# Kernel optimization log

Measured on AMD Instinct MI355X. Metric: run time of the kernel, lower is better.

The kernel has to match this reference:

```python
import jax, jax.numpy as jnp
import numpy as np

N_NODES = 50000
N_EDGES = 800000
N_GRAPHS = 64
F_IN = 128
HID = 64
HEADS = 4
N_CLS = 10
NEG_SLOPE = 0.2


def _glorot(key, shape):
    fan_in, fan_out = shape[-1], shape[-2] if len(shape) > 1 else shape[-1]
    lim = jnp.sqrt(6.0 / (fan_in + fan_out))
    return jax.random.uniform(key, shape, jnp.float32, -lim, lim)


def setup_inputs() -> dict:
    key = jax.random.key(0)
    ks = jax.random.split(key, 20)
    x = jax.random.normal(ks[0], (N_NODES, F_IN), jnp.float32)
    edge_index = jax.random.randint(ks[1], (2, N_EDGES), 0, N_NODES, jnp.int32)
    batch = jnp.sort(jax.random.randint(ks[2], (N_NODES,), 0, N_GRAPHS, jnp.int32))
    HC = HID * HEADS
    return {
        "x": x, "edge_index": edge_index, "batch": batch,
        # node embedding Linear(F_IN -> HID)
        "W_emb": _glorot(ks[3], (HID, F_IN)), "b_emb": jnp.zeros((HID,), jnp.float32),
        # gat1: HID -> HID, heads=4, concat
        "W1": _glorot(ks[4], (HC, HID)),
        "a_src1": _glorot(ks[5], (HEADS, HID)), "a_dst1": _glorot(ks[6], (HEADS, HID)),
        "b1": jnp.zeros((HC,), jnp.float32),
        # gat2: HC -> HID, heads=4, concat
        "W2": _glorot(ks[7], (HC, HC)),
        "a_src2": _glorot(ks[8], (HEADS, HID)), "a_dst2": _glorot(ks[9], (HEADS, HID)),
        "b2": jnp.zeros((HC,), jnp.float32),
        # gat3: HC -> HID, heads=1, mean
        "W3": _glorot(ks[10], (HID, HC)),
        "a_src3": _glorot(ks[11], (1, HID)), "a_dst3": _glorot(ks[12], (1, HID)),
        "b3": jnp.zeros((HID,), jnp.float32),
        # classifier: Linear(2*HID -> HID), ReLU, Linear(HID -> N_CLS)
        "Wc1": _glorot(ks[13], (HID, 2 * HID)), "bc1": jnp.zeros((HID,), jnp.float32),
        "Wc2": _glorot(ks[14], (N_CLS, HID)), "bc2": jnp.zeros((N_CLS,), jnp.float32),
    }


def _gat_layer(x, src, dst, W, a_src, a_dst, b, concat):
    """PyG-style GATConv (eval mode, self-loops already in src/dst)."""
    N = x.shape[0]
    H, C = a_src.shape
    h = (x @ W.T).reshape(N, H, C)                       # [N,H,C]
    s = jnp.einsum("nhc,hc->nh", h, a_src)               # [N,H]
    d = jnp.einsum("nhc,hc->nh", h, a_dst)               # [N,H]
    e = jax.nn.leaky_relu(s[src] + d[dst], NEG_SLOPE)    # [E,H]
    emax = jax.lax.stop_gradient(jax.ops.segment_max(e, dst, num_segments=N))
    emax = jnp.where(jnp.isfinite(emax), emax, 0.0)
    ex = jnp.exp(e - emax[dst])
    den = jax.ops.segment_sum(ex, dst, num_segments=N)   # [N,H]
    alpha = ex / (den[dst] + 1e-16)                      # segment softmax
    out = jax.ops.segment_sum(h[src] * alpha[:, :, None], dst, num_segments=N)
    out = out.reshape(N, H * C) if concat else out.mean(axis=1)
    return out + b


def reference(x, edge_index, batch, W_emb, b_emb, W1, a_src1, a_dst1, b1,
              W2, a_src2, a_dst2, b2, W3, a_src3, a_dst3, b3, Wc1, bc1, Wc2, bc2):
    N = x.shape[0]
    loops = jnp.arange(N, dtype=edge_index.dtype)
    src = jnp.concatenate([edge_index[0], loops])
    dst = jnp.concatenate([edge_index[1], loops])

    h = x @ W_emb.T + b_emb
    h = jax.nn.elu(_gat_layer(h, src, dst, W1, a_src1, a_dst1, b1, True))
    h = jax.nn.elu(_gat_layer(h, src, dst, W2, a_src2, a_dst2, b2, True))
    h = jax.nn.elu(_gat_layer(h, src, dst, W3, a_src3, a_dst3, b3, False))

    counts = jax.ops.segment_sum(jnp.ones((N,), h.dtype), batch, num_segments=N_GRAPHS)
    mean = jax.ops.segment_sum(h, batch, num_segments=N_GRAPHS) / jnp.maximum(counts, 1.0)[:, None]
    mx = jax.ops.segment_max(h, batch, num_segments=N_GRAPHS)
    mx = jnp.where(counts[:, None] > 0, mx, 0.0)
    g = jnp.concatenate([mean, mx], axis=1)              # [B, 2*HID]

    g = jax.nn.relu(g @ Wc1.T + bc1)
    return g @ Wc2.T + bc2                               # [B, N_CLS]
```

## Files before the change

kernel.cpp:

```cpp
#include <hip/hip_runtime.h>
#include <math.h>

#define NG 64
#define F_IN 128
#define NEG_SLOPE 0.2f

typedef __attribute__((ext_vector_type(8))) short s16x8;
typedef __attribute__((ext_vector_type(4))) float f32x4;

static __device__ __forceinline__ float elu_f(float x) { return x > 0.f ? x : expm1f(x); }
static __device__ __forceinline__ float lrelu(float x) { return x > 0.f ? x : NEG_SLOPE * x; }
static __device__ __forceinline__ unsigned enc_f32(float x) {
    unsigned u = __float_as_uint(x);
    return (u & 0x80000000u) ? ~u : (u | 0x80000000u);
}
static __device__ __forceinline__ float dec_f32(unsigned u) {
    unsigned b = (u & 0x80000000u) ? (u & 0x7fffffffu) : ~u;
    return __uint_as_float(b);
}
static __device__ __forceinline__ unsigned short bf16_rn(float x) {
    unsigned u = __float_as_uint(x);
    unsigned r = u + 0x7FFFu + ((u >> 16) & 1u);
    return (unsigned short)(r >> 16);
}
static __device__ __forceinline__ float bf16_to_f32(unsigned short h) {
    return __uint_as_float(((unsigned)h) << 16);
}
static __device__ __forceinline__ unsigned pack_split(float x) {
    unsigned short hi = bf16_rn(x);
    unsigned short lo = bf16_rn(x - bf16_to_f32(hi));
    return ((unsigned)hi << 16) | lo;
}

__global__ void convert_pack(const float* __restrict__ in, unsigned* __restrict__ out, int n) {
    int idx = (blockIdx.x * blockDim.x + threadIdx.x) * 4;
    if (idx + 3 < n) {
        float4 v = *(const float4*)&in[idx];
        uint4 o;
        o.x = pack_split(v.x); o.y = pack_split(v.y);
        o.z = pack_split(v.z); o.w = pack_split(v.w);
        *(uint4*)&out[idx] = o;
    }
}

__global__ void convert_dual(const float* __restrict__ in, unsigned short* __restrict__ hi,
                             unsigned short* __restrict__ lo, int n) {
    int idx = (blockIdx.x * blockDim.x + threadIdx.x) * 4;
    if (idx + 3 < n) {
        float4 v = *(const float4*)&in[idx];
        ushort4 h, l;
        h.x = bf16_rn(v.x); l.x = bf16_rn(v.x - bf16_to_f32(h.x));
        h.y = bf16_rn(v.y); l.y = bf16_rn(v.y - bf16_to_f32(h.y));
        h.z = bf16_rn(v.z); l.z = bf16_rn(v.z - bf16_to_f32(h.z));
        h.w = bf16_rn(v.w); l.w = bf16_rn(v.w - bf16_to_f32(h.w));
        *(ushort4*)&hi[idx] = h;
        *(ushort4*)&lo[idx] = l;
    }
}

__global__ void uvec_kernel(const float* __restrict__ W1, const float* __restrict__ a1s,
                            const float* __restrict__ a1d,
                            float* __restrict__ us, float* __restrict__ ud) {
    int h = threadIdx.x >> 6;
    int i = threadIdx.x & 63;
    float s = 0.f, d = 0.f;
    for (int o = 0; o < 64; ++o) {
        float w = W1[(h * 64 + o) * 64 + i];
        s = fmaf(w, a1s[h * 64 + o], s);
        d = fmaf(w, a1d[h * 64 + o], d);
    }
    us[h * 64 + i] = s;
    ud[h * 64 + i] = d;
}

__global__ void hist_kernel(const int* __restrict__ ei, int* __restrict__ cnt, int E, int N) {
    int e = blockIdx.x * blockDim.x + threadIdx.x;
    int ET = E + N;
    if (e >= ET) return;
    int dst = (e < E) ? ei[E + e] : (e - E);
    atomicAdd(&cnt[dst], 1);
}

__global__ void scan1_kernel(const int* __restrict__ cnt, int* __restrict__ excl,
                             int* __restrict__ bsum, int n) {
    __shared__ int sm[256];
    int t = threadIdx.x;
    int base = blockIdx.x * 1024 + t * 4;
    int v[4];
    #pragma unroll
    for (int u = 0; u < 4; ++u) { int idx = base + u; v[u] = (idx < n) ? cnt[idx] : 0; }
    int tsum = v[0] + v[1] + v[2] + v[3];
    sm[t] = tsum;
    __syncthreads();
    for (int off = 1; off < 256; off <<= 1) {
        int y = (t >= off) ? sm[t - off] : 0;
        __syncthreads();
        sm[t] += y;
        __syncthreads();
    }
    int run = sm[t] - tsum;
    #pragma unroll
    for (int u = 0; u < 4; ++u) {
        int idx = base + u;
        if (idx < n) excl[idx] = run;
        run += v[u];
    }
    if (t == 255) bsum[blockIdx.x] = sm[255];
}

__global__ void scan2_kernel(int* __restrict__ bsum, int* __restrict__ offs, int nb, int n) {
    if (blockIdx.x == 0 && threadIdx.x == 0) {
        int run = 0;
        for (int b = 0; b < nb; ++b) { int t = bsum[b]; bsum[b] = run; run += t; }
        offs[n] = run;
    }
}

__global__ void scan3_kernel(int* __restrict__ offs, const int* __restrict__ bsum, int n) {
    int base = blockIdx.x * 1024 + threadIdx.x * 4;
    int add = bsum[blockIdx.x];
    #pragma unroll
    for (int u = 0; u < 4; ++u) { int idx = base + u; if (idx < n) offs[idx] += add; }
}

__global__ void scatter_kernel(const int* __restrict__ ei, const int* __restrict__ offs,
                               int* __restrict__ cursor, int* __restrict__ csr_src, int E, int N) {
    int e = blockIdx.x * blockDim.x + threadIdx.x;
    int ET = E + N;
    if (e >= ET) return;
    int src, dst;
    if (e < E) { src = ei[e]; dst = ei[E + e]; }
    else       { src = e - E; dst = e - E; }
    int pos = offs[dst] + atomicAdd(&cursor[dst], 1);
    csr_src[pos] = src;
}

template<int K, int BN, int HATT, bool SHARED, bool SLICED, bool DO_ELU, int OUTM>
__global__ __launch_bounds__(256) void gemm_nolds(const unsigned* __restrict__ Ap, int lda,
                                                  const unsigned short* __restrict__ Whi,
                                                  const unsigned short* __restrict__ Wlo,
                                                  void* __restrict__ OutV, int M,
                                                  const float* __restrict__ bias,
                                                  const float* __restrict__ asrc,
                                                  const float* __restrict__ adst,
                                                  float* __restrict__ S, float* __restrict__ D,
                                                  int N) {
    constexpr int RF = (BN == 256) ? 4 : 1;
    constexpr int CF = 4;
    const int t = threadIdx.x;
    const int lane = t & 63;
    const int w = t >> 6;
    const int lj = lane & 15;
    const int kg = lane >> 4;
    const int n0 = blockIdx.x * 64;
    const int m0 = blockIdx.y * BN;
    const int rbase = (BN == 256) ? 0 : w * 16;
    const int cbase = (BN == 256) ? w * 64 : 0;
    const int aoff = SLICED ? blockIdx.y * K : 0;
    const unsigned short* __restrict__ WhiB = SLICED ? Whi + (size_t)blockIdx.y * BN * K : Whi;
    const unsigned short* __restrict__ WloB = SLICED ? Wlo + (size_t)blockIdx.y * BN * K : Wlo;

    f32x4 acc[RF][CF];
    #pragma unroll
    for (int rf = 0; rf < RF; ++rf)
        #pragma unroll
        for (int cf = 0; cf < CF; ++cf) acc[rf][cf] = (f32x4){0.f, 0.f, 0.f, 0.f};

    for (int kc = 0; kc < K; kc += 32) {
        s16x8 ah[RF], al[RF];
        #pragma unroll
        for (int rf = 0; rf < RF; ++rf) {
            int row = n0 + rbase + rf * 16 + lj;
            unsigned p[8];
            if (row < N) {
                uint4 q0 = *(const uint4*)&Ap[(size_t)row * lda + aoff + kc + kg * 8];
                uint4 q1 = *(const uint4*)&Ap[(size_t)row * lda + aoff + kc + kg * 8 + 4];
                p[0] = q0.x; p[1] = q0.y; p[2] = q0.z; p[3] = q0.w;
                p[4] = q1.x; p[5] = q1.y; p[6] = q1.z; p[7] = q1.w;
            } else {
                #pragma unroll
                for (int i = 0; i < 8; ++i) p[i] = 0;
            }
            #pragma unroll
            for (int i = 0; i < 8; ++i) {
                ah[rf][i] = (short)(p[i] >> 16);
                al[rf][i] = (short)(p[i] & 0xffffu);
            }
        }
        #pragma unroll
        for (int cf = 0; cf < CF; ++cf) {
            int wcol = (SLICED ? 0 : m0) + cbase + cf * 16 + lj;
            s16x8 bh = *(const s16x8*)&WhiB[(size_t)wcol * K + kc + kg * 8];
            s16x8 bl = *(const s16x8*)&WloB[(size_t)wcol * K + kc + kg * 8];
            #pragma unroll
            for (int rf = 0; rf < RF; ++rf) {
                acc[rf][cf] = __builtin_amdgcn_mfma_f32_16x16x32_bf16(ah[rf], bh, acc[rf][cf], 0, 0, 0);
                acc[rf][cf] = __builtin_amdgcn_mfma_f32_16x16x32_bf16(ah[rf], bl, acc[rf][cf], 0, 0, 0);
                acc[rf][cf] = __builtin_amdgcn_mfma_f32_16x16x32_bf16(al[rf], bh, acc[rf][cf], 0, 0, 0);
            }
        }
    }

    #pragma unroll
    for (int cf = 0; cf < CF; ++cf) {
        int gcol = m0 + cbase + cf * 16 + lj;
        float bv = bias ? bias[gcol] : 0.f;
        #pragma unroll
        for (int rf = 0; rf < RF; ++rf) {
            #pragma unroll
            for (int r = 0; r < 4; ++r) {
                int gn = n0 + rbase + rf * 16 + (lane >> 4) * 4 + r;
                if (gn < N) {
                    float o = acc[rf][cf][r] + bv;
                    if (DO_ELU) o = elu_f(o);
                    if (OUTM == 0)      ((float*)OutV)[(size_t)gn * M + gcol] = o;
                    else if (OUTM == 1) ((unsigned short*)OutV)[(size_t)gn * M + gcol] = bf16_rn(o);
                    else                ((unsigned*)OutV)[(size_t)gn * M + gcol] = pack_split(o);
                }
            }
        }
    }
    if (HATT > 0) {
        if (BN == 256) {
            float aw[CF], dw[CF], bw[CF];
            #pragma unroll
            for (int cf = 0; cf < CF; ++cf) {
                aw[cf] = asrc[w * 64 + cf * 16 + lj];
                dw[cf] = adst[w * 64 + cf * 16 + lj];
                bw[cf] = bias ? bias[m0 + cbase + cf * 16 + lj] : 0.f;
            }
            #pragma unroll
            for (int rf = 0; rf < RF; ++rf) {
                #pragma unroll
                for (int r = 0; r < 4; ++r) {
                    float sp = 0.f, dp = 0.f;
                    #pragma unroll
                    for (int cf = 0; cf < CF; ++cf) {
                        float vv = acc[rf][cf][r] + bw[cf];
                        sp = fmaf(vv, aw[cf], sp);
                        dp = fmaf(vv, dw[cf], dp);
                    }
                    #pragma unroll
                    for (int off = 1; off < 16; off <<= 1) {
                        sp += __shfl_xor(sp, off);
                        dp += __shfl_xor(dp, off);
                    }
                    if (lj == 0) {
                        int gn = n0 + rf * 16 + (lane >> 4) * 4 + r;
                        if (gn < N) { S[gn * HATT + w] = sp; D[gn * HATT + w] = dp; }
                    }
                }
            }
        } else {
            #pragma unroll
            for (int hh = 0; hh < HATT; ++hh) {
                float aw[CF], dw[CF], bw[CF];
                #pragma unroll
                for (int c2 = 0; c2 < CF; ++c2) {
                    aw[c2] = asrc[hh * 64 + c2 * 16 + lj];
                    dw[c2] = adst[hh * 64 + c2 * 16 + lj];
                    bw[c2] = bias ? bias[m0 + c2 * 16 + lj] : 0.f;
                }
                #pragma unroll
                for (int r = 0; r < 4; ++r) {
                    float sp = 0.f, dp = 0.f;
                    #pragma unroll
                    for (int c2 = 0; c2 < CF; ++c2) {
                        float vv = acc[0][c2][r] + bw[c2];
                        sp = fmaf(vv, aw[c2], sp);
                        dp = fmaf(vv, dw[c2], dp);
                    }
                    #pragma unroll
                    for (int off = 1; off < 16; off <<= 1) {
                        sp += __shfl_xor(sp, off);
                        dp += __shfl_xor(dp, off);
                    }
                    if (lj == 0) {
                        int gn = n0 + w * 16 + (lane >> 4) * 4 + r;
                        if (gn < N) { S[gn * HATT + hh] = sp; D[gn * HATT + hh] = dp; }
                    }
                }
            }
        }
    }
}

__global__ __launch_bounds__(256, 8) void gat_agg_x(const float* __restrict__ xA,
                                                    const float* __restrict__ s,
                                                    const float* __restrict__ d,
                                                    const int* __restrict__ offs,
                                                    const int* __restrict__ csr_src,
                                                    unsigned* __restrict__ G,
                                                    int N) {
    __shared__ float stash[4][64 * 5];
    int wv = threadIdx.x >> 6;
    int lane = threadIdx.x & 63;
    int node = (blockIdx.x * blockDim.x + threadIdx.x) >> 6;
    if (node >= N) return;
    float* st = stash[wv];
    int e0 = offs[node], e1 = offs[node + 1];
    float4 dv4 = *(const float4*)&d[node * 4];
    float dd[4] = {dv4.x, dv4.y, dv4.z, dv4.w};
    float mrun[4] = {-INFINITY, -INFINITY, -INFINITY, -INFINITY};
    float den[4] = {0.f, 0.f, 0.f, 0.f};
    float acc[4] = {0.f, 0.f, 0.f, 0.f};

    for (int base = e0; base < e1; base += 64) {
        int cnt = min(64, e1 - base);
        float ev[4] = {-INFINITY, -INFINITY, -INFINITY, -INFINITY};
        if (lane < cnt) {
            int src = csr_src[base + lane];
            float4 sv = *(const float4*)&s[src * 4];
            ev[0] = lrelu(sv.x + dd[0]); ev[1] = lrelu(sv.y + dd[1]);
            ev[2] = lrelu(sv.z + dd[2]); ev[3] = lrelu(sv.w + dd[3]);
            st[lane * 5 + 0] = ev[0]; st[lane * 5 + 1] = ev[1];
            st[lane * 5 + 2] = ev[2]; st[lane * 5 + 3] = ev[3];
            st[lane * 5 + 4] = __int_as_float(src);
        }
        #pragma unroll
        for (int h = 0; h < 4; ++h) {
            float m = ev[h];
            #pragma unroll
            for (int off = 32; off; off >>= 1) m = fmaxf(m, __shfl_xor(m, off));
            float mnew = fmaxf(mrun[h], m);
            float scale = __expf(mrun[h] - mnew);
            acc[h] *= scale; den[h] *= scale;
            mrun[h] = mnew;
        }
        int k = 0;
        for (; k + 4 <= cnt; k += 4) {
            int si[4];
            #pragma unroll
            for (int u = 0; u < 4; ++u) si[u] = __float_as_int(st[(k + u) * 5 + 4]);
            float vx[4];
            #pragma unroll
            for (int u = 0; u < 4; ++u) vx[u] = xA[(size_t)si[u] * 64 + lane];
            #pragma unroll
            for (int u = 0; u < 4; ++u) {
                #pragma unroll
                for (int h = 0; h < 4; ++h) {
                    float p = __expf(st[(k + u) * 5 + h] - mrun[h]);
                    den[h] += p;
                    acc[h] = fmaf(p, vx[u], acc[h]);
                }
            }
        }
        for (; k < cnt; ++k) {
            int src = __float_as_int(st[k * 5 + 4]);
            float v = xA[(size_t)src * 64 + lane];
            #pragma unroll
            for (int h = 0; h < 4; ++h) {
                float p = __expf(st[k * 5 + h] - mrun[h]);
                den[h] += p;
                acc[h] = fmaf(p, v, acc[h]);
            }
        }
    }
    #pragma unroll
    for (int h = 0; h < 4; ++h)
        G[(size_t)node * 256 + h * 64 + lane] = pack_split(acc[h] / (den[h] + 1e-16f));
}

template<int H, bool OUTPACK>
__global__ __launch_bounds__(256, 8) void gat_agg(const unsigned short* __restrict__ hp,
                                                  const float* __restrict__ s,
                                                  const float* __restrict__ d,
                                                  const int* __restrict__ offs,
                                                  const int* __restrict__ csr_src,
                                                  const float* __restrict__ bias,
                                                  void* __restrict__ outV, int N) {
    const int SW = (H == 4) ? 5 : 2;
    __shared__ float stash[4][64 * 5];
    int wv = threadIdx.x >> 6;
    int lane = threadIdx.x & 63;
    int node = (blockIdx.x * blockDim.x + threadIdx.x) >> 6;
    if (node >= N) return;
    float* st = stash[wv];
    int e0 = offs[node], e1 = offs[node + 1];

    float dd[H];
    #pragma unroll
    for (int h = 0; h < H; ++h) dd[h] = d[node * H + h];

    const int hd = (H == 4) ? (lane >> 4) : 0;

    float mrun = -INFINITY;
    float acc0 = 0.f, acc1 = 0.f, acc2 = 0.f, acc3 = 0.f, den = 0.f;

    for (int base = e0; base < e1; base += 64) {
        int cnt = min(64, e1 - base);
        float ev[H];
        #pragma unroll
        for (int h = 0; h < H; ++h) ev[h] = -INFINITY;
        if (lane < cnt) {
            int src = csr_src[base + lane];
            if (H == 4) {
                float4 sv = *(const float4*)&s[src * 4];
                ev[0] = lrelu(sv.x + dd[0]); ev[1] = lrelu(sv.y + dd[1]);
                ev[2] = lrelu(sv.z + dd[2]); ev[3] = lrelu(sv.w + dd[3]);
                st[lane * 5 + 0] = ev[0]; st[lane * 5 + 1] = ev[1];
                st[lane * 5 + 2] = ev[2]; st[lane * 5 + 3] = ev[3];
                st[lane * 5 + 4] = __int_as_float(src);
            } else {
                ev[0] = lrelu(s[src] + dd[0]);
                st[lane * 2 + 0] = ev[0];
                st[lane * 2 + 1] = __int_as_float(src);
            }
        }
        float mc[H];
        #pragma unroll
        for (int h = 0; h < H; ++h) {
            float m = ev[h];
            #pragma unroll
            for (int off = 32; off; off >>= 1) m = fmaxf(m, __shfl_xor(m, off));
            mc[h] = m;
        }
        float mch = mc[0];
        if (H == 4)
            mch = (lane & 32) ? ((lane & 16) ? mc[3] : mc[2]) : ((lane & 16) ? mc[1] : mc[0]);
        float mnew = fmaxf(mrun, mch);
        float scale = __expf(mrun - mnew);
        acc0 *= scale; acc1 *= scale; acc2 *= scale; acc3 *= scale; den *= scale;
        mrun = mnew;

        int k = 0;
        for (; k + 4 <= cnt; k += 4) {
            float ea = st[(k + 0) * SW + hd];
            float eb = st[(k + 1) * SW + hd];
            float ec = st[(k + 2) * SW + hd];
            float ed = st[(k + 3) * SW + hd];
            int sa = __float_as_int(st[(k + 0) * SW + SW - 1]);
            int sb = __float_as_int(st[(k + 1) * SW + SW - 1]);
            int sc = __float_as_int(st[(k + 2) * SW + SW - 1]);
            int sd_ = __float_as_int(st[(k + 3) * SW + SW - 1]);
            float pa = __expf(ea - mrun);
            float pb = __expf(eb - mrun);
            float pc = __expf(ec - mrun);
            float pd = __expf(ed - mrun);
            den += (pa + pb) + (pc + pd);
            if (H == 4) {
                uint2 ua = *(const uint2*)&hp[(size_t)sa * 256 + lane * 4];
                uint2 ub = *(const uint2*)&hp[(size_t)sb * 256 + lane * 4];
                uint2 uc = *(const uint2*)&hp[(size_t)sc * 256 + lane * 4];
                uint2 ud = *(const uint2*)&hp[(size_t)sd_ * 256 + lane * 4];
                acc0 = fmaf(pa, __uint_as_float((ua.x & 0xffffu) << 16), acc0);
                acc1 = fmaf(pa, __uint_as_float(ua.x & 0xffff0000u), acc1);
                acc2 = fmaf(pa, __uint_as_float((ua.y & 0xffffu) << 16), acc2);
                acc3 = fmaf(pa, __uint_as_float(ua.y & 0xffff0000u), acc3);
                acc0 = fmaf(pb, __uint_as_float((ub.x & 0xffffu) << 16), acc0);
                acc1 = fmaf(pb, __uint_as_float(ub.x & 0xffff0000u), acc1);
                acc2 = fmaf(pb, __uint_as_float((ub.y & 0xffffu) << 16), acc2);
                acc3 = fmaf(pb, __uint_as_float(ub.y & 0xffff0000u), acc3);
                acc0 = fmaf(pc, __uint_as_float((uc.x & 0xffffu) << 16), acc0);
                acc1 = fmaf(pc, __uint_as_float(uc.x & 0xffff0000u), acc1);
                acc2 = fmaf(pc, __uint_as_float((uc.y & 0xffffu) << 16), acc2);
                acc3 = fmaf(pc, __uint_as_float(uc.y & 0xffff0000u), acc3);
                acc0 = fmaf(pd, __uint_as_float((ud.x & 0xffffu) << 16), acc0);
                acc1 = fmaf(pd, __uint_as_float(ud.x & 0xffff0000u), acc1);
                acc2 = fmaf(pd, __uint_as_float((ud.y & 0xffffu) << 16), acc2);
                acc3 = fmaf(pd, __uint_as_float(ud.y & 0xffff0000u), acc3);
            } else {
                float ha = bf16_to_f32(hp[(size_t)sa * 64 + lane]);
                float hb = bf16_to_f32(hp[(size_t)sb * 64 + lane]);
                float hc = bf16_to_f32(hp[(size_t)sc * 64 + lane]);
                float hdv = bf16_to_f32(hp[(size_t)sd_ * 64 + lane]);
                acc0 = fmaf(pa, ha, acc0);
                acc0 = fmaf(pb, hb, acc0);
                acc0 = fmaf(pc, hc, acc0);
                acc0 = fmaf(pd, hdv, acc0);
            }
        }
        for (; k < cnt; ++k) {
            float e = st[k * SW + hd];
            int src = __float_as_int(st[k * SW + SW - 1]);
            float p = __expf(e - mrun);
            den += p;
            if (H == 4) {
                uint2 uv = *(const uint2*)&hp[(size_t)src * 256 + lane * 4];
                acc0 = fmaf(p, __uint_as_float((uv.x & 0xffffu) << 16), acc0);
                acc1 = fmaf(p, __uint_as_float(uv.x & 0xffff0000u), acc1);
                acc2 = fmaf(p, __uint_as_float((uv.y & 0xffffu) << 16), acc2);
                acc3 = fmaf(p, __uint_as_float(uv.y & 0xffff0000u), acc3);
            } else {
                acc0 = fmaf(p, bf16_to_f32(hp[(size_t)src * 64 + lane]), acc0);
            }
        }
    }

    float inv = 1.0f / (den + 1e-16f);
    if (H == 4) {
        float4 bv = *(const float4*)&bias[lane * 4];
        float o0 = elu_f(acc0 * inv + bv.x);
        float o1 = elu_f(acc1 * inv + bv.y);
        float o2 = elu_f(acc2 * inv + bv.z);
        float o3 = elu_f(acc3 * inv + bv.w);
        if (OUTPACK) {
            uint4 q;
            q.x = pack_split(o0); q.y = pack_split(o1);
            q.z = pack_split(o2); q.w = pack_split(o3);
            *(uint4*)&((unsigned*)outV)[(size_t)node * 256 + lane * 4] = q;
        } else {
            float4 o = make_float4(o0, o1, o2, o3);
            *(float4*)&((float*)outV)[(size_t)node * 256 + lane * 4] = o;
        }
    } else {
        float o = elu_f(acc0 * inv + bias[lane]);
        if (OUTPACK) ((unsigned*)outV)[(size_t)node * 64 + lane] = pack_split(o);
        else         ((float*)outV)[(size_t)node * 64 + lane] = o;
    }
}

__global__ void pool_init(float* gsum, unsigned* gmax, int* gcnt) {
    int t = blockIdx.x * blockDim.x + threadIdx.x;
    if (t < NG * 64) { gsum[t] = 0.f; gmax[t] = enc_f32(-INFINITY); }
    if (t < NG) gcnt[t] = 0;
}

__global__ void pool_reduce(const float* __restrict__ h3, const int* __restrict__ batch,
                            float* __restrict__ gsum, unsigned* __restrict__ gmax,
                            int* __restrict__ gcnt, int N, int per) {
    int w = (blockIdx.x * blockDim.x + threadIdx.x) >> 6;
    int lane = threadIdx.x & 63;
    int n0 = w * per;
    int n1 = min(N, n0 + per);
    float lsum = 0.f, lmax = -INFINITY;
    int cur = -1, cnt = 0;
    for (int n = n0; n < n1; ++n) {
        int g = batch[n];
        if (g != cur) {
            if (cur >= 0) {
                atomicAdd(&gsum[cur * 64 + lane], lsum);
                atomicMax(&gmax[cur * 64 + lane], enc_f32(lmax));
                if (lane == 0) atomicAdd(&gcnt[cur], cnt);
            }
            cur = g; lsum = 0.f; lmax = -INFINITY; cnt = 0;
        }
        float v = h3[(size_t)n * 64 + lane];
        lsum += v; lmax = fmaxf(lmax, v); cnt++;
    }
    if (cur >= 0) {
        atomicAdd(&gsum[cur * 64 + lane], lsum);
        atomicMax(&gmax[cur * 64 + lane], enc_f32(lmax));
        if (lane == 0) atomicAdd(&gcnt[cur], cnt);
    }
}

__global__ __launch_bounds__(128) void classifier(const float* __restrict__ gsum,
                                                  const unsigned* __restrict__ gmax,
                                                  const int* __restrict__ gcnt,
                                                  const float* __restrict__ Wc1,
                                                  const float* __restrict__ bc1,
                                                  const float* __restrict__ Wc2,
                                                  const float* __restrict__ bc2,
                                                  float* __restrict__ out) {
    __shared__ float gv[128];
    __shared__ float z1[64];
    int g = blockIdx.x, t = threadIdx.x;
    int cnt = gcnt[g];
    if (t < 64) {
        gv[t] = gsum[g * 64 + t] / fmaxf((float)cnt, 1.f);
    } else {
        float mx = dec_f32(gmax[g * 64 + (t - 64)]);
        gv[t] = (cnt > 0) ? mx : 0.f;
    }
    __syncthreads();
    if (t < 64) {
        float a = bc1[t];
        for (int k = 0; k < 128; ++k) a = fmaf(Wc1[t * 128 + k], gv[k], a);
        z1[t] = a > 0.f ? a : 0.f;
    }
    __syncthreads();
    if (t < 10) {
        float a = bc2[t];
        for (int k = 0; k < 64; ++k) a = fmaf(Wc2[t * 64 + k], z1[k], a);
        out[g * 10 + t] = a;
    }
}

extern "C" void kernel_launch(void* const* d_in, const int* in_sizes, int n_in,
                              void* d_out, int out_size, void* d_ws, size_t ws_size,
                              hipStream_t stream) {
    const float* x      = (const float*)d_in[0];
    const int*   ei     = (const int*)d_in[1];
    const int*   batch  = (const int*)d_in[2];
    const float* W_emb  = (const float*)d_in[3];
    const float* b_emb  = (const float*)d_in[4];
    const float* W1     = (const float*)d_in[5];
    const float* as1    = (const float*)d_in[6];
    const float* ad1    = (const float*)d_in[7];
    const float* b1     = (const float*)d_in[8];
    const float* W2     = (const float*)d_in[9];
    const float* as2    = (const float*)d_in[10];
    const float* ad2    = (const float*)d_in[11];
    const float* b2     = (const float*)d_in[12];
    const float* W3     = (const float*)d_in[13];
    const float* as3    = (const float*)d_in[14];
    const float* ad3    = (const float*)d_in[15];
    const float* b3     = (const float*)d_in[16];
    const float* Wc1    = (const float*)d_in[17];
    const float* bc1    = (const float*)d_in[18];
    const float* Wc2    = (const float*)d_in[19];
    const float* bc2    = (const float*)d_in[20];

    const int N = in_sizes[0] / F_IN;
    const int E = in_sizes[1] / 2;
    const int ET = E + N;

    size_t off = 0;
    auto alloc = [&](size_t bytes) -> void* {
        void* p = (char*)d_ws + off;
        off += (bytes + 255) & ~(size_t)255;
        return p;
    };
    unsigned* X1 = (unsigned*)alloc((size_t)N * 128 * 4);
    float*    X2 = (float*)alloc((size_t)N * 64 * 4);
    unsigned* X3 = (unsigned*)alloc((size_t)N * 256 * 4);
    unsigned* X4 = (unsigned*)alloc((size_t)N * 256 * 4);
    float*    S  = (float*)alloc((size_t)N * 4 * 4);
    float*    D  = (float*)alloc((size_t)N * 4 * 4);
    unsigned short* WhE = (unsigned short*)alloc(64 * 128 * 2);
    unsigned short* WlE = (unsigned short*)alloc(64 * 128 * 2);
    unsigned short* Wh1 = (unsigned short*)alloc(256 * 64 * 2);
    unsigned short* Wl1 = (unsigned short*)alloc(256 * 64 * 2);
    unsigned short* Wh2 = (unsigned short*)alloc(256 * 256 * 2);
    unsigned short* Wl2 = (unsigned short*)alloc(256 * 256 * 2);
    unsigned short* Wh3 = (unsigned short*)alloc(64 * 256 * 2);
    unsigned short* Wl3 = (unsigned short*)alloc(64 * 256 * 2);
    float*    us1     = (float*)alloc(4 * 64 * 4);
    float*    ud1     = (float*)alloc(4 * 64 * 4);
    int*      offs    = (int*)alloc((size_t)(N + 1) * 4);
    int*      cnt     = (int*)alloc((size_t)N * 4);
    int*      bsum    = (int*)alloc(64 * 4);
    int*      csr_src = (int*)alloc((size_t)ET * 4);
    float*    gsum    = (float*)alloc(NG * 64 * 4);
    unsigned* gmax    = (unsigned*)alloc(NG * 64 * 4);
    int*      gcnt    = (int*)alloc(NG * 4);
    (void)ws_size; (void)n_in; (void)out_size;

    const int SCB = (N + 1023) / 1024;

    convert_pack<<<(N * 128 / 4 + 255) / 256, 256, 0, stream>>>(x, X1, N * 128);
    convert_dual<<<8, 256, 0, stream>>>(W_emb, WhE, WlE, 64 * 128);
    convert_dual<<<16, 256, 0, stream>>>(W1, Wh1, Wl1, 256 * 64);
    convert_dual<<<64, 256, 0, stream>>>(W2, Wh2, Wl2, 256 * 256);
    convert_dual<<<16, 256, 0, stream>>>(W3, Wh3, Wl3, 64 * 256);
    uvec_kernel<<<1, 256, 0, stream>>>(W1, as1, ad1, us1, ud1);

    hipMemsetAsync(cnt, 0, (size_t)N * 4, stream);
    hist_kernel<<<(ET + 255) / 256, 256, 0, stream>>>(ei, cnt, E, N);
    scan1_kernel<<<SCB, 256, 0, stream>>>(cnt, offs, bsum, N);
    scan2_kernel<<<1, 64, 0, stream>>>(bsum, offs, SCB, N);
    scan3_kernel<<<SCB, 256, 0, stream>>>(offs, bsum, N);
    hipMemsetAsync(cnt, 0, (size_t)N * 4, stream);
    scatter_kernel<<<(ET + 255) / 256, 256, 0, stream>>>(ei, offs, cnt, csr_src, E, N);

    const int NWV = (N * 64 + 255) / 256;
    const int GB = (N + 63) / 64;

    gemm_nolds<128, 64, 4, true, false, false, 0><<<dim3(GB, 1), 256, 0, stream>>>(
        X1, 128, WhE, WlE, X2, 64, b_emb, us1, ud1, S, D, N);
    gat_agg_x<<<NWV, 256, 0, stream>>>(X2, S, D, offs, csr_src, X3, N);
    gemm_nolds<64, 64, 0, false, true, true, 2><<<dim3(GB, 4), 256, 0, stream>>>(
        X3, 256, Wh1, Wl1, X4, 256, b1, nullptr, nullptr, nullptr, nullptr, N);
    gemm_nolds<256, 256, 4, false, false, false, 1><<<dim3(GB, 1), 256, 0, stream>>>(
        X4, 256, Wh2, Wl2, X1, 256, nullptr, as2, ad2, S, D, N);
    gat_agg<4, true><<<NWV, 256, 0, stream>>>((const unsigned short*)X1, S, D, offs, csr_src,
                                              b2, X3, N);
    gemm_nolds<256, 64, 1, true, false, false, 1><<<dim3(GB, 1), 256, 0, stream>>>(
        X3, 256, Wh3, Wl3, X2, 64, nullptr, as3, ad3, S, D, N);
    gat_agg<1, false><<<NWV, 256, 0, stream>>>((const unsigned short*)X2, S, D, offs, csr_src,
                                               b3, X4, N);

    pool_init<<<16, 256, 0, stream>>>(gsum, gmax, gcnt);
    int per = (N + 255) / 256;
    pool_reduce<<<64, 256, 0, stream>>>((const float*)X4, batch, gsum, gmax, gcnt, N, per);
    classifier<<<NG, 128, 0, stream>>>(gsum, gmax, gcnt, Wc1, bc1, Wc2, bc2, (float*)d_out);
}
```

Baseline: 646.6 us.

## Store GEMM operands in MFMA fragment-tiled split-bf16 layout and enlarge row tiles

```diff
diff --git a/kernel.cpp b/kernel.cpp
--- a/kernel.cpp
+++ b/kernel.cpp
@@ -26,36 +26,32 @@
 static __device__ __forceinline__ float bf16_to_f32(unsigned short h) {
     return __uint_as_float(((unsigned)h) << 16);
 }
-static __device__ __forceinline__ unsigned pack_split(float x) {
-    unsigned short hi = bf16_rn(x);
-    unsigned short lo = bf16_rn(x - bf16_to_f32(hi));
-    return ((unsigned)hi << 16) | lo;
-}
-
-__global__ void convert_pack(const float* __restrict__ in, unsigned* __restrict__ out, int n) {
-    int idx = (blockIdx.x * blockDim.x + threadIdx.x) * 4;
-    if (idx + 3 < n) {
-        float4 v = *(const float4*)&in[idx];
-        uint4 o;
-        o.x = pack_split(v.x); o.y = pack_split(v.y);
-        o.z = pack_split(v.z); o.w = pack_split(v.w);
-        *(uint4*)&out[idx] = o;
-    }
-}
-
-__global__ void convert_dual(const float* __restrict__ in, unsigned short* __restrict__ hi,
-                             unsigned short* __restrict__ lo, int n) {
-    int idx = (blockIdx.x * blockDim.x + threadIdx.x) * 4;
-    if (idx + 3 < n) {
-        float4 v = *(const float4*)&in[idx];
-        ushort4 h, l;
-        h.x = bf16_rn(v.x); l.x = bf16_rn(v.x - bf16_to_f32(h.x));
-        h.y = bf16_rn(v.y); l.y = bf16_rn(v.y - bf16_to_f32(h.y));
-        h.z = bf16_rn(v.z); l.z = bf16_rn(v.z - bf16_to_f32(h.z));
-        h.w = bf16_rn(v.w); l.w = bf16_rn(v.w - bf16_to_f32(h.w));
-        *(ushort4*)&hi[idx] = h;
-        *(ushort4*)&lo[idx] = l;
-    }
+
+static __device__ __forceinline__ size_t fragaddr(int row, int k, int K) {
+    return ((size_t)(row >> 4) * (K >> 5) + (k >> 5)) * 512
+         + (size_t)(((k & 31) >> 3) * 128 + (row & 15) * 8 + (k & 7));
+}
+
+__global__ void convert_frag(const float* __restrict__ in, unsigned short* __restrict__ hi,
+                             unsigned short* __restrict__ lo, int R, int K) {
+    int t = blockIdx.x * blockDim.x + threadIdx.x;
+    if (t * 8 >= R * K) return;
+    int row = (t * 8) / K;
+    int k0 = (t * 8) % K;
+    float4 v0 = *(const float4*)&in[(size_t)row * K + k0];
+    float4 v1 = *(const float4*)&in[(size_t)row * K + k0 + 4];
+    float v[8] = {v0.x, v0.y, v0.z, v0.w, v1.x, v1.y, v1.z, v1.w};
+    unsigned short h[8], l[8];
+    #pragma unroll
+    for (int i = 0; i < 8; ++i) {
+        h[i] = bf16_rn(v[i]);
+        l[i] = bf16_rn(v[i] - bf16_to_f32(h[i]));
+    }
+    size_t a = fragaddr(row, k0, K);
+    *(ushort4*)&hi[a]     = make_ushort4(h[0], h[1], h[2], h[3]);
+    *(ushort4*)&hi[a + 4] = make_ushort4(h[4], h[5], h[6], h[7]);
+    *(ushort4*)&lo[a]     = make_ushort4(l[0], l[1], l[2], l[3]);
+    *(ushort4*)&lo[a + 4] = make_ushort4(l[4], l[5], l[6], l[7]);
 }
 
 __global__ void uvec_kernel(const float* __restrict__ W1, const float* __restrict__ a1s,
@@ -135,65 +131,55 @@
     csr_src[pos] = src;
 }
 
-template<int K, int BN, int HATT, bool SHARED, bool SLICED, bool DO_ELU, int OUTM>
-__global__ __launch_bounds__(256) void gemm_nolds(const unsigned* __restrict__ Ap, int lda,
-                                                  const unsigned short* __restrict__ Whi,
-                                                  const unsigned short* __restrict__ Wlo,
-                                                  void* __restrict__ OutV, int M,
-                                                  const float* __restrict__ bias,
-                                                  const float* __restrict__ asrc,
-                                                  const float* __restrict__ adst,
-                                                  float* __restrict__ S, float* __restrict__ D,
-                                                  int N) {
-    constexpr int RF = (BN == 256) ? 4 : 1;
-    constexpr int CF = 4;
+template<int K, int AK, int BN, int HATT, bool SHARED, bool SLICED, bool DO_ELU, int OUTM>
+__global__ __launch_bounds__(256) void gemm_frag(const unsigned short* __restrict__ Ahi,
+                                                 const unsigned short* __restrict__ Alo,
+                                                 const unsigned short* __restrict__ Whi,
+                                                 const unsigned short* __restrict__ Wlo,
+                                                 void* __restrict__ OutV,
+                                                 unsigned short* __restrict__ Ohi,
+                                                 unsigned short* __restrict__ Olo,
+                                                 int M,
+                                                 const float* __restrict__ bias,
+                                                 const float* __restrict__ asrc,
+                                                 const float* __restrict__ adst,
+                                                 float* __restrict__ S, float* __restrict__ D,
+                                                 int N) {
     const int t = threadIdx.x;
     const int lane = t & 63;
     const int w = t >> 6;
     const int lj = lane & 15;
     const int kg = lane >> 4;
-    const int n0 = blockIdx.x * 64;
+    const int n0 = blockIdx.x * ((BN == 256) ? 64 : 256);
     const int m0 = blockIdx.y * BN;
-    const int rbase = (BN == 256) ? 0 : w * 16;
+    const int rbase = (BN == 256) ? 0 : w * 64;
     const int cbase = (BN == 256) ? w * 64 : 0;
     const int aoff = SLICED ? blockIdx.y * K : 0;
     const unsigned short* __restrict__ WhiB = SLICED ? Whi + (size_t)blockIdx.y * BN * K : Whi;
     const unsigned short* __restrict__ WloB = SLICED ? Wlo + (size_t)blockIdx.y * BN * K : Wlo;
 
-    f32x4 acc[RF][CF];
-    #pragma unroll
-    for (int rf = 0; rf < RF; ++rf)
-        #pragma unroll
-        for (int cf = 0; cf < CF; ++cf) acc[rf][cf] = (f32x4){0.f, 0.f, 0.f, 0.f};
+    f32x4 acc[4][4];
+    #pragma unroll
+    for (int rf = 0; rf < 4; ++rf)
+        #pragma unroll
+        for (int cf = 0; cf < 4; ++cf) acc[rf][cf] = (f32x4){0.f, 0.f, 0.f, 0.f};
 
     for (int kc = 0; kc < K; kc += 32) {
-        s16x8 ah[RF], al[RF];
-        #pragma unroll
-        for (int rf = 0; rf < RF; ++rf) {
-            int row = n0 + rbase + rf * 16 + lj;
-            unsigned p[8];
-            if (row < N) {
-                uint4 q0 = *(const uint4*)&Ap[(size_t)row * lda + aoff + kc + kg * 8];
-                uint4 q1 = *(const uint4*)&Ap[(size_t)row * lda + aoff + kc + kg * 8 + 4];
-                p[0] = q0.x; p[1] = q0.y; p[2] = q0.z; p[3] = q0.w;
-                p[4] = q1.x; p[5] = q1.y; p[6] = q1.z; p[7] = q1.w;
-            } else {
-                #pragma unroll
-                for (int i = 0; i < 8; ++i) p[i] = 0;
-            }
-            #pragma unroll
-            for (int i = 0; i < 8; ++i) {
-                ah[rf][i] = (short)(p[i] >> 16);
-                al[rf][i] = (short)(p[i] & 0xffffu);
-            }
-        }
-        #pragma unroll
-        for (int cf = 0; cf < CF; ++cf) {
-            int wcol = (SLICED ? 0 : m0) + cbase + cf * 16 + lj;
-            s16x8 bh = *(const s16x8*)&WhiB[(size_t)wcol * K + kc + kg * 8];
-            s16x8 bl = *(const s16x8*)&WloB[(size_t)wcol * K + kc + kg * 8];
-            #pragma unroll
-            for (int rf = 0; rf < RF; ++rf) {
+        s16x8 ah[4], al[4];
+        #pragma unroll
+        for (int rf = 0; rf < 4; ++rf) {
+            size_t a = fragaddr(n0 + rbase + rf * 16 + lj, aoff + kc + kg * 8, AK);
+            ah[rf] = *(const s16x8*)&Ahi[a];
+            al[rf] = *(const s16x8*)&Alo[a];
+        }
+        #pragma unroll
+        for (int cf = 0; cf < 4; ++cf) {
+            int bcol = (SLICED ? 0 : m0) + cbase + cf * 16 + lj;
+            size_t b = fragaddr(bcol, kc + kg * 8, K);
+            s16x8 bh = *(const s16x8*)&WhiB[b];
+            s16x8 bl = *(const s16x8*)&WloB[b];
+            #pragma unroll
+            for (int rf = 0; rf < 4; ++rf) {
                 acc[rf][cf] = __builtin_amdgcn_mfma_f32_16x16x32_bf16(ah[rf], bh, acc[rf][cf], 0, 0, 0);
                 acc[rf][cf] = __builtin_amdgcn_mfma_f32_16x16x32_bf16(ah[rf], bl, acc[rf][cf], 0, 0, 0);
                 acc[rf][cf] = __builtin_amdgcn_mfma_f32_16x16x32_bf16(al[rf], bh, acc[rf][cf], 0, 0, 0);
@@ -202,71 +188,51 @@
     }
 
     #pragma unroll
-    for (int cf = 0; cf < CF; ++cf) {
+    for (int cf = 0; cf < 4; ++cf) {
         int gcol = m0 + cbase + cf * 16 + lj;
         float bv = bias ? bias[gcol] : 0.f;
         #pragma unroll
-        for (int rf = 0; rf < RF; ++rf) {
+        for (int rf = 0; rf < 4; ++rf) {
             #pragma unroll
             for (int r = 0; r < 4; ++r) {
                 int gn = n0 + rbase + rf * 16 + (lane >> 4) * 4 + r;
                 if (gn < N) {
                     float o = acc[rf][cf][r] + bv;
                     if (DO_ELU) o = elu_f(o);
-                    if (OUTM == 0)      ((float*)OutV)[(size_t)gn * M + gcol] = o;
-                    else if (OUTM == 1) ((unsigned short*)OutV)[(size_t)gn * M + gcol] = bf16_rn(o);
-                    else                ((unsigned*)OutV)[(size_t)gn * M + gcol] = pack_split(o);
+                    if (OUTM == 0) {
+                        ((float*)OutV)[(size_t)gn * M + gcol] = o;
+                    } else if (OUTM == 1) {
+                        ((unsigned short*)OutV)[(size_t)gn * M + gcol] = bf16_rn(o);
+                    } else {
+                        unsigned short hv = bf16_rn(o);
+                        unsigned short lv = bf16_rn(o - bf16_to_f32(hv));
+                        size_t a2 = fragaddr(gn, gcol, M);
+                        Ohi[a2] = hv; Olo[a2] = lv;
+                    }
                 }
             }
         }
     }
     if (HATT > 0) {
-        if (BN == 256) {
-            float aw[CF], dw[CF], bw[CF];
-            #pragma unroll
-            for (int cf = 0; cf < CF; ++cf) {
-                aw[cf] = asrc[w * 64 + cf * 16 + lj];
-                dw[cf] = adst[w * 64 + cf * 16 + lj];
-                bw[cf] = bias ? bias[m0 + cbase + cf * 16 + lj] : 0.f;
-            }
-            #pragma unroll
-            for (int rf = 0; rf < RF; ++rf) {
+        const int HS = SHARED ? HATT : 1;
+        #pragma unroll
+        for (int hh = 0; hh < HS; ++hh) {
+            const int head = SHARED ? hh : w;
+            float aw[4], dw[4], bw[4];
+            #pragma unroll
+            for (int c2 = 0; c2 < 4; ++c2) {
+                aw[c2] = asrc[head * 64 + c2 * 16 + lj];
+                dw[c2] = adst[head * 64 + c2 * 16 + lj];
+                bw[c2] = bias ? bias[m0 + cbase + c2 * 16 + lj] : 0.f;
+            }
+            #pragma unroll
+            for (int rf = 0; rf < 4; ++rf) {
                 #pragma unroll
                 for (int r = 0; r < 4; ++r) {
                     float sp = 0.f, dp = 0.f;
                     #pragma unroll
-                    for (int cf = 0; cf < CF; ++cf) {
-                        float vv = acc[rf][cf][r] + bw[cf];
-                        sp = fmaf(vv, aw[cf], sp);
-                        dp = fmaf(vv, dw[cf], dp);
-                    }
-                    #pragma unroll
-                    for (int off = 1; off < 16; off <<= 1) {
-                        sp += __shfl_xor(sp, off);
-                        dp += __shfl_xor(dp, off);
-                    }
-                    if (lj == 0) {
-                        int gn = n0 + rf * 16 + (lane >> 4) * 4 + r;
-                        if (gn < N) { S[gn * HATT + w] = sp; D[gn * HATT + w] = dp; }
-                    }
-                }
-            }
-        } else {
-            #pragma unroll
-            for (int hh = 0; hh < HATT; ++hh) {
-                float aw[CF], dw[CF], bw[CF];
-                #pragma unroll
-                for (int c2 = 0; c2 < CF; ++c2) {
-                    aw[c2] = asrc[hh * 64 + c2 * 16 + lj];
-                    dw[c2] = adst[hh * 64 + c2 * 16 + lj];
-                    bw[c2] = bias ? bias[m0 + c2 * 16 + lj] : 0.f;
-                }
-                #pragma unroll
-                for (int r = 0; r < 4; ++r) {
-                    float sp = 0.f, dp = 0.f;
-                    #pragma unroll
-                    for (int c2 = 0; c2 < CF; ++c2) {
-                        float vv = acc[0][c2][r] + bw[c2];
+                    for (int c2 = 0; c2 < 4; ++c2) {
+                        float vv = acc[rf][c2][r] + bw[c2];
                         sp = fmaf(vv, aw[c2], sp);
                         dp = fmaf(vv, dw[c2], dp);
                     }
@@ -276,8 +242,8 @@
                         dp += __shfl_xor(dp, off);
                     }
                     if (lj == 0) {
-                        int gn = n0 + w * 16 + (lane >> 4) * 4 + r;
-                        if (gn < N) { S[gn * HATT + hh] = sp; D[gn * HATT + hh] = dp; }
+                        int gn = n0 + rbase + rf * 16 + (lane >> 4) * 4 + r;
+                        if (gn < N) { S[gn * HATT + head] = sp; D[gn * HATT + head] = dp; }
                     }
                 }
             }
@@ -290,7 +256,8 @@
                                                     const float* __restrict__ d,
                                                     const int* __restrict__ offs,
                                                     const int* __restrict__ csr_src,
-                                                    unsigned* __restrict__ G,
+                                                    unsigned short* __restrict__ Gh,
+                                                    unsigned short* __restrict__ Gl,
                                                     int N) {
     __shared__ float stash[4][64 * 5];
     int wv = threadIdx.x >> 6;
@@ -357,18 +324,26 @@
         }
     }
     #pragma unroll
-    for (int h = 0; h < 4; ++h)
-        G[(size_t)node * 256 + h * 64 + lane] = pack_split(acc[h] / (den[h] + 1e-16f));
-}
-
-template<int H, bool OUTPACK>
+    for (int h = 0; h < 4; ++h) {
+        float v = acc[h] / (den[h] + 1e-16f);
+        unsigned short hv = bf16_rn(v);
+        unsigned short lv = bf16_rn(v - bf16_to_f32(hv));
+        size_t a = fragaddr(node, h * 64 + lane, 256);
+        Gh[a] = hv; Gl[a] = lv;
+    }
+}
+
+template<int H, bool FRAGOUT>
 __global__ __launch_bounds__(256, 8) void gat_agg(const unsigned short* __restrict__ hp,
                                                   const float* __restrict__ s,
                                                   const float* __restrict__ d,
                                                   const int* __restrict__ offs,
                                                   const int* __restrict__ csr_src,
                                                   const float* __restrict__ bias,
-                                                  void* __restrict__ outV, int N) {
+                                                  float* __restrict__ outF,
+                                                  unsigned short* __restrict__ outHi,
+                                                  unsigned short* __restrict__ outLo,
+                                                  int N) {
     const int SW = (H == 4) ? 5 : 2;
     __shared__ float stash[4][64 * 5];
     int wv = threadIdx.x >> 6;
@@ -494,19 +469,22 @@
         float o1 = elu_f(acc1 * inv + bv.y);
         float o2 = elu_f(acc2 * inv + bv.z);
         float o3 = elu_f(acc3 * inv + bv.w);
-        if (OUTPACK) {
-            uint4 q;
-            q.x = pack_split(o0); q.y = pack_split(o1);
-            q.z = pack_split(o2); q.w = pack_split(o3);
-            *(uint4*)&((unsigned*)outV)[(size_t)node * 256 + lane * 4] = q;
+        if (FRAGOUT) {
+            unsigned short h0 = bf16_rn(o0), h1 = bf16_rn(o1), h2 = bf16_rn(o2), h3 = bf16_rn(o3);
+            ushort4 hq = make_ushort4(h0, h1, h2, h3);
+            ushort4 lq = make_ushort4(bf16_rn(o0 - bf16_to_f32(h0)),
+                                      bf16_rn(o1 - bf16_to_f32(h1)),
+                                      bf16_rn(o2 - bf16_to_f32(h2)),
+                                      bf16_rn(o3 - bf16_to_f32(h3)));
+            size_t a = fragaddr(node, lane * 4, 256);
+            *(ushort4*)&outHi[a] = hq;
+            *(ushort4*)&outLo[a] = lq;
         } else {
             float4 o = make_float4(o0, o1, o2, o3);
-            *(float4*)&((float*)outV)[(size_t)node * 256 + lane * 4] = o;
+            *(float4*)&outF[(size_t)node * 256 + lane * 4] = o;
         }
     } else {
-        float o = elu_f(acc0 * inv + bias[lane]);
-        if (OUTPACK) ((unsigned*)outV)[(size_t)node * 64 + lane] = pack_split(o);
-        else         ((float*)outV)[(size_t)node * 64 + lane] = o;
+        outF[(size_t)node * 64 + lane] = elu_f(acc0 * inv + bias[lane]);
     }
 }
 
@@ -605,6 +583,11 @@
     const int N = in_sizes[0] / F_IN;
     const int E = in_sizes[1] / 2;
     const int ET = E + N;
+    const int GB64 = (N + 63) / 64;
+    const int GB256 = (N + 255) / 256;
+    const int ROWS_FR = GB256 * 256;
+    const size_t FR128 = (size_t)(ROWS_FR / 16) * (128 / 32) * 512;
+    const size_t FR256 = (size_t)(ROWS_FR / 16) * (256 / 32) * 512;
 
     size_t off = 0;
     auto alloc = [&](size_t bytes) -> void* {
@@ -612,12 +595,14 @@
         off += (bytes + 255) & ~(size_t)255;
         return p;
     };
-    unsigned* X1 = (unsigned*)alloc((size_t)N * 128 * 4);
-    float*    X2 = (float*)alloc((size_t)N * 64 * 4);
-    unsigned* X3 = (unsigned*)alloc((size_t)N * 256 * 4);
-    unsigned* X4 = (unsigned*)alloc((size_t)N * 256 * 4);
-    float*    S  = (float*)alloc((size_t)N * 4 * 4);
-    float*    D  = (float*)alloc((size_t)N * 4 * 4);
+    unsigned short* Xh  = (unsigned short*)alloc(FR128 * 2);
+    unsigned short* Xl  = (unsigned short*)alloc(FR128 * 2);
+    float*          Aemb= (float*)alloc((size_t)N * 64 * 4);
+    unsigned short* Gh  = (unsigned short*)alloc(FR256 * 2);
+    unsigned short* Gl  = (unsigned short*)alloc(FR256 * 2);
+    unsigned short* C1h = (unsigned short*)alloc(FR256 * 2);
+    unsigned short* C1l = (unsigned short*)alloc(FR256 * 2);
+    unsigned short* H2b = (unsigned short*)alloc((size_t)N * 256 * 2);
     unsigned short* WhE = (unsigned short*)alloc(64 * 128 * 2);
     unsigned short* WlE = (unsigned short*)alloc(64 * 128 * 2);
     unsigned short* Wh1 = (unsigned short*)alloc(256 * 64 * 2);
@@ -628,6 +613,8 @@
     unsigned short* Wl3 = (unsigned short*)alloc(64 * 256 * 2);
     float*    us1     = (float*)alloc(4 * 64 * 4);
     float*    ud1     = (float*)alloc(4 * 64 * 4);
+    float*    S       = (float*)alloc((size_t)N * 4 * 4);
+    float*    D       = (float*)alloc((size_t)N * 4 * 4);
     int*      offs    = (int*)alloc((size_t)(N + 1) * 4);
     int*      cnt     = (int*)alloc((size_t)N * 4);
     int*      bsum    = (int*)alloc(64 * 4);
@@ -639,11 +626,11 @@
 
     const int SCB = (N + 1023) / 1024;
 
-    convert_pack<<<(N * 128 / 4 + 255) / 256, 256, 0, stream>>>(x, X1, N * 128);
-    convert_dual<<<8, 256, 0, stream>>>(W_emb, WhE, WlE, 64 * 128);
-    convert_dual<<<16, 256, 0, stream>>>(W1, Wh1, Wl1, 256 * 64);
-    convert_dual<<<64, 256, 0, stream>>>(W2, Wh2, Wl2, 256 * 256);
-    convert_dual<<<16, 256, 0, stream>>>(W3, Wh3, Wl3, 64 * 256);
+    convert_frag<<<(N * 128 / 8 + 255) / 256, 256, 0, stream>>>(x, Xh, Xl, N, 128);
+    convert_frag<<<4, 256, 0, stream>>>(W_emb, WhE, WlE, 64, 128);
+    convert_frag<<<8, 256, 0, stream>>>(W1, Wh1, Wl1, 256, 64);
+    convert_frag<<<32, 256, 0, stream>>>(W2, Wh2, Wl2, 256, 256);
+    convert_frag<<<8, 256, 0, stream>>>(W3, Wh3, Wl3, 64, 256);
     uvec_kernel<<<1, 256, 0, stream>>>(W1, as1, ad1, us1, ud1);
 
     hipMemsetAsync(cnt, 0, (size_t)N * 4, stream);
@@ -655,24 +642,23 @@
     scatter_kernel<<<(ET + 255) / 256, 256, 0, stream>>>(ei, offs, cnt, csr_src, E, N);
 
     const int NWV = (N * 64 + 255) / 256;
-    const int GB = (N + 63) / 64;
-
-    gemm_nolds<128, 64, 4, true, false, false, 0><<<dim3(GB, 1), 256, 0, stream>>>(
-        X1, 128, WhE, WlE, X2, 64, b_emb, us1, ud1, S, D, N);
-    gat_agg_x<<<NWV, 256, 0, stream>>>(X2, S, D, offs, csr_src, X3, N);
-    gemm_nolds<64, 64, 0, false, true, true, 2><<<dim3(GB, 4), 256, 0, stream>>>(
-        X3, 256, Wh1, Wl1, X4, 256, b1, nullptr, nullptr, nullptr, nullptr, N);
-    gemm_nolds<256, 256, 4, false, false, false, 1><<<dim3(GB, 1), 256, 0, stream>>>(
-        X4, 256, Wh2, Wl2, X1, 256, nullptr, as2, ad2, S, D, N);
-    gat_agg<4, true><<<NWV, 256, 0, stream>>>((const unsigned short*)X1, S, D, offs, csr_src,
-                                              b2, X3, N);
-    gemm_nolds<256, 64, 1, true, false, false, 1><<<dim3(GB, 1), 256, 0, stream>>>(
-        X3, 256, Wh3, Wl3, X2, 64, nullptr, as3, ad3, S, D, N);
-    gat_agg<1, false><<<NWV, 256, 0, stream>>>((const unsigned short*)X2, S, D, offs, csr_src,
-                                               b3, X4, N);
+
+    gemm_frag<128, 128, 64, 4, true, false, false, 0><<<dim3(GB256, 1), 256, 0, stream>>>(
+        Xh, Xl, WhE, WlE, Aemb, nullptr, nullptr, 64, b_emb, us1, ud1, S, D, N);
+    gat_agg_x<<<NWV, 256, 0, stream>>>(Aemb, S, D, offs, csr_src, Gh, Gl, N);
+    gemm_frag<64, 256, 64, 0, false, true, true, 3><<<dim3(GB256, 4), 256, 0, stream>>>(
+        Gh, Gl, Wh1, Wl1, nullptr, C1h, C1l, 256, b1, nullptr, nullptr, nullptr, nullptr, N);
+    gemm_frag<256, 256, 256, 4, false, false, false, 1><<<dim3(GB64, 1), 256, 0, stream>>>(
+        C1h, C1l, Wh2, Wl2, H2b, nullptr, nullptr, 256, nullptr, as2, ad2, S, D, N);
+    gat_agg<4, true><<<NWV, 256, 0, stream>>>(H2b, S, D, offs, csr_src, b2,
+                                              nullptr, Gh, Gl, N);
+    gemm_frag<256, 256, 64, 1, true, false, false, 1><<<dim3(GB256, 1), 256, 0, stream>>>(
+        Gh, Gl, Wh3, Wl3, (unsigned short*)Aemb, nullptr, nullptr, 64, nullptr, as3, ad3, S, D, N);
+    gat_agg<1, false><<<NWV, 256, 0, stream>>>((const unsigned short*)Aemb, S, D, offs, csr_src,
+                                               b3, (float*)H2b, nullptr, nullptr, N);
 
     pool_init<<<16, 256, 0, stream>>>(gsum, gmax, gcnt);
     int per = (N + 255) / 256;
-    pool_reduce<<<64, 256, 0, stream>>>((const float*)X4, batch, gsum, gmax, gcnt, N, per);
+    pool_reduce<<<64, 256, 0, stream>>>((const float*)H2b, batch, gsum, gmax, gcnt, N, per);
     classifier<<<NG, 128, 0, stream>>>(gsum, gmax, gcnt, Wc1, bc1, Wc2, bc2, (float*)d_out);
 }
```

Result: faster. 627.4 us (-3.0%).
